# Kernel tuning notes

Measured on AMD Instinct MI355X. Metric: run time of the kernel, lower is better.

## Reference

```python
import jax, jax.numpy as jnp
import numpy as np


def setup_inputs() -> dict:
    key = jax.random.key(0)
    k1, k2, k3 = jax.random.split(key, 3)
    b, n, d, f = 16, 2048, 256, 256
    features = jax.random.normal(k1, (b, n, d), dtype=jnp.float32)
    # dense adjacency; row-normalize like MeanAggregator's normalized A
    A = jax.random.uniform(k2, (b, n, n), dtype=jnp.float32)
    A = A / jnp.sum(A, axis=-1, keepdims=True)
    weight = jax.random.normal(k3, (2 * d, f), dtype=jnp.float32) * (1.0 / np.sqrt(2 * d))
    bias = jnp.zeros((f,), dtype=jnp.float32)
    return {"features": features, "A": A, "weight": weight, "bias": bias}


def reference(features, A, weight, bias):
    # agg = A @ features  (MeanAggregator: row-normalized adjacency)
    agg = jnp.einsum('bnm,bmd->bnd', A, features)  # [b,n,d]
    d = features.shape[-1]
    # split-weight GEMM instead of materializing concat:
    # [feat, agg] @ W == feat @ W[:d] + agg @ W[d:]
    out = (jnp.einsum('bnd,df->bnf', features, weight[:d])
           + jnp.einsum('bnd,df->bnf', agg, weight[d:])
           + bias)
    return jax.nn.relu(out)
```

## Files before the change

kernel.cpp:

```cpp
#include <hip/hip_runtime.h>

typedef __attribute__((ext_vector_type(8))) short bf16x8;
typedef __attribute__((ext_vector_type(4))) float f32x4;

__device__ __forceinline__ unsigned short f2bf(float f) {
    unsigned int u = __builtin_bit_cast(unsigned int, f);
    unsigned int r = (u + 0x7FFFu + ((u >> 16) & 1u)) >> 16;
    return (unsigned short)r;
}
__device__ __forceinline__ unsigned int pkbf(float lo, float hi) {
    unsigned int ul = __builtin_bit_cast(unsigned int, lo) + 0x8000u;
    unsigned int uh = __builtin_bit_cast(unsigned int, hi) + 0x8000u;
    return (uh & 0xFFFF0000u) | (ul >> 16);
}
__device__ __forceinline__ float bf2f(unsigned short u) {
    unsigned int x = ((unsigned int)u) << 16;
    return __builtin_bit_cast(float, x);
}

__device__ __forceinline__ void gll16(const void* g, void* l) {
    __builtin_amdgcn_global_load_lds(
        (const __attribute__((address_space(1))) void*)g,
        (__attribute__((address_space(3))) void*)l, 16, 0, 0);
}

__global__ __launch_bounds__(256) void transpose_cvt_kernel(
    const float* __restrict__ src, unsigned short* __restrict__ dstT,
    unsigned short* __restrict__ dstS, int R, int C)
{
    __shared__ float tile[64][65];
    const int b = blockIdx.z;
    const float* s = src + (size_t)b * R * C;
    const int r0 = blockIdx.x * 64, c0 = blockIdx.y * 64;
    const int t = threadIdx.x;
    const int r = t >> 2, cg = (t & 3) * 16;

    float v[16];
    const float4* p = reinterpret_cast<const float4*>(s + (size_t)(r0 + r) * C + c0 + cg);
#pragma unroll
    for (int i = 0; i < 4; ++i) {
        float4 q = p[i];
        v[4 * i + 0] = q.x; v[4 * i + 1] = q.y; v[4 * i + 2] = q.z; v[4 * i + 3] = q.w;
    }
#pragma unroll
    for (int i = 0; i < 16; ++i) tile[r][cg + i] = v[i];

    if (dstS) {
        unsigned int w[8];
#pragma unroll
        for (int i = 0; i < 8; ++i)
            w[i] = (unsigned)f2bf(v[2 * i]) | ((unsigned)f2bf(v[2 * i + 1]) << 16);
        unsigned int* d = reinterpret_cast<unsigned int*>(
            dstS + (size_t)b * R * C + (size_t)(r0 + r) * C + c0 + cg);
        *reinterpret_cast<uint4*>(d)     = make_uint4(w[0], w[1], w[2], w[3]);
        *reinterpret_cast<uint4*>(d + 4) = make_uint4(w[4], w[5], w[6], w[7]);
    }

    __syncthreads();

    const int cl = t >> 2, rg = (t & 3) * 16;
    unsigned int w[8];
#pragma unroll
    for (int i = 0; i < 8; ++i) {
        unsigned short lo = f2bf(tile[rg + 2 * i][cl]);
        unsigned short hi = f2bf(tile[rg + 2 * i + 1][cl]);
        w[i] = (unsigned)lo | ((unsigned)hi << 16);
    }
    unsigned int* d = reinterpret_cast<unsigned int*>(
        dstT + (size_t)b * R * C + (size_t)(c0 + cl) * R + r0 + rg);
    *reinterpret_cast<uint4*>(d)     = make_uint4(w[0], w[1], w[2], w[3]);
    *reinterpret_cast<uint4*>(d + 4) = make_uint4(w[4], w[5], w[6], w[7]);
}

__global__ __launch_bounds__(256, 2) void kpre_gemm(
    const float* __restrict__ F, const unsigned short* __restrict__ Wt,
    const float* __restrict__ bias, unsigned short* __restrict__ H,
    unsigned short* __restrict__ Gt)
{
    __shared__ __align__(16) short Fb[64 * 256];
    __shared__ __align__(16) short Wb[256 * 64];

    const int tid = threadIdx.x;
    const int lane = tid & 63, wid = tid >> 6;
    const int lo = lane & 15, hi = lane >> 4;
    const int rb = blockIdx.x;
    const int batch = rb >> 5;
    const int mb = (rb & 31) * 64;
    const size_t m0g = (size_t)rb * 64;

    {
        const int frow = tid >> 2, fq = tid & 3;
        const float* fp = F + (m0g + frow) * 256 + fq * 64;
#pragma unroll
        for (int g = 0; g < 2; ++g) {
            float4 q[8];
#pragma unroll
            for (int i = 0; i < 8; ++i)
                q[i] = reinterpret_cast<const float4*>(fp)[g * 8 + i];
#pragma unroll
            for (int j = 0; j < 4; ++j) {
                unsigned int w0 = pkbf(q[2*j].x,   q[2*j].y);
                unsigned int w1 = pkbf(q[2*j].z,   q[2*j].w);
                unsigned int w2 = pkbf(q[2*j+1].x, q[2*j+1].y);
                unsigned int w3 = pkbf(q[2*j+1].z, q[2*j+1].w);
                int slot = fq * 8 + g * 4 + j;
                int off = frow * 256 + ((slot ^ (frow & 7)) << 3);
                *reinterpret_cast<uint4*>(&Fb[off]) = make_uint4(w0, w1, w2, w3);
            }
        }
    }

    f32x4 acc[4][4];

#pragma unroll
    for (int pass = 0; pass < 2; ++pass) {
#pragma unroll
        for (int m = 0; m < 4; ++m)
#pragma unroll
            for (int n = 0; n < 4; ++n) acc[m][n] = (f32x4){0.f, 0.f, 0.f, 0.f};

        for (int kt = 0; kt < 4; ++kt) {
            const int kbase = pass * 256 + kt * 64;
#pragma unroll
            for (int it = 0; it < 8; ++it) {
                int si = it * 256 + tid;
                int row = si >> 3, slot = si & 7;
                const unsigned short* g = Wt + (size_t)row * 512 + kbase + ((slot ^ (row & 7)) << 3);
                gll16(g, Wb + (size_t)si * 8);
            }
            __syncthreads();

#pragma unroll
            for (int kk = 0; kk < 2; ++kk) {
                bf16x8 af[4], bw[4];
#pragma unroll
                for (int m = 0; m < 4; ++m) {
                    int row = m * 16 + lo;
                    int slot = kt * 8 + kk * 4 + hi;
                    af[m] = *reinterpret_cast<const bf16x8*>(&Fb[row * 256 + ((slot ^ (row & 7)) << 3)]);
                }
#pragma unroll
                for (int n = 0; n < 4; ++n) {
                    int row = wid * 64 + n * 16 + lo;
                    bw[n] = *reinterpret_cast<const bf16x8*>(&Wb[row * 64 + (((kk * 4 + hi) ^ (row & 7)) << 3)]);
                }
#pragma unroll
                for (int m = 0; m < 4; ++m)
#pragma unroll
                    for (int n = 0; n < 4; ++n)
                        acc[m][n] = __builtin_amdgcn_mfma_f32_16x16x32_bf16(af[m], bw[n], acc[m][n], 0, 0, 0);
            }
            __syncthreads();
        }

        if (pass == 0) {
            float bv[4];
#pragma unroll
            for (int n = 0; n < 4; ++n) bv[n] = bias[wid * 64 + n * 16 + lo];
            unsigned short* Hb = H + m0g * 256;
#pragma unroll
            for (int m = 0; m < 4; ++m)
#pragma unroll
                for (int n = 0; n < 4; ++n)
#pragma unroll
                    for (int j = 0; j < 4; ++j) {
                        int row = m * 16 + hi * 4 + j;
                        int col = wid * 64 + n * 16 + lo;
                        Hb[(size_t)row * 256 + col] = f2bf(acc[m][n][j] + bv[n]);
                    }
        } else {
            short* T = Wb + wid * 4096;
#pragma unroll
            for (int m = 0; m < 4; ++m)
#pragma unroll
                for (int n = 0; n < 4; ++n)
#pragma unroll
                    for (int j = 0; j < 4; ++j) {
                        int gr = m * 16 + hi * 4 + j;
                        int gc = n * 16 + lo;
                        int slot = gr >> 3, e = gr & 7;
                        T[gc * 64 + ((slot ^ (gc & 7)) << 3) + e] = f2bf(acc[m][n][j]);
                    }
            unsigned short* Gb = Gt + ((size_t)batch * 256 + wid * 64) * 2048 + mb;
#pragma unroll
            for (int i = 0; i < 8; ++i) {
                int f = i * 8 + (lane >> 3);
                int s = lane & 7;
                bf16x8 v = *reinterpret_cast<const bf16x8*>(&T[f * 64 + ((s ^ (f & 7)) << 3)]);
                *reinterpret_cast<bf16x8*>(Gb + (size_t)f * 2048 + s * 8) = v;
            }
        }
    }
}

__global__ __launch_bounds__(512) void kmain_gemm(
    const float* __restrict__ A, const unsigned short* __restrict__ Gt,
    unsigned short* __restrict__ P)
{
    __shared__ __align__(16) short Ab[2][256 * 64];
    __shared__ __align__(16) short Bb[2][256 * 64];

    const int tid = threadIdx.x;
    const int lane = tid & 63, wid = tid >> 6;
    const int wr = wid >> 2, wc = wid & 3;
    const int lo = lane & 15, hi = lane >> 4;

    const int bid = blockIdx.x;
    const int wg = ((bid & 7) << 5) | (bid >> 3);
    const int batch = wg >> 4;
    const int ks    = (wg >> 3) & 1;
    const int mt    = wg & 7;

    const float* Abase = A + ((size_t)batch * 2048 + (size_t)mt * 256) * 2048 + (size_t)ks * 1024;
    const unsigned short* Gbase = Gt + (size_t)batch * 256 * 2048 + (size_t)ks * 1024;

    const int arow = tid >> 1;
    const int ac0  = (tid & 1) * 32;

    f32x4 acc[8][4];
#pragma unroll
    for (int m = 0; m < 8; ++m)
#pragma unroll
        for (int n = 0; n < 4; ++n) acc[m][n] = (f32x4){0.f, 0.f, 0.f, 0.f};

    float4 qa[8];
    auto loadA = [&](int k0) {
        const float4* p = reinterpret_cast<const float4*>(
            Abase + (size_t)arow * 2048 + k0 + ac0);
#pragma unroll
        for (int i = 0; i < 8; ++i) qa[i] = p[i];
    };
    auto writeA = [&](int buf) {
#pragma unroll
        for (int j = 0; j < 4; ++j) {
            uint4 w;
            w.x = pkbf(qa[2*j].x,   qa[2*j].y);
            w.y = pkbf(qa[2*j].z,   qa[2*j].w);
            w.z = pkbf(qa[2*j+1].x, qa[2*j+1].y);
            w.w = pkbf(qa[2*j+1].z, qa[2*j+1].w);
            int slot = (tid & 1) * 4 + j;
            int off = arow * 64 + ((slot ^ (arow & 7)) << 3);
            *reinterpret_cast<uint4*>(&Ab[buf][off]) = w;
        }
    };
    auto stageB = [&](int buf, int k0) {
#pragma unroll
        for (int it = 0; it < 4; ++it) {
            int si = it * 512 + tid;
            int row = si >> 3, slot = si & 7;
            const unsigned short* g = Gbase + (size_t)row * 2048 + k0 + ((slot ^ (row & 7)) << 3);
            gll16(g, &Bb[buf][(size_t)si * 8]);
        }
    };
    auto compute = [&](int buf) {
#pragma unroll
        for (int kk = 0; kk < 2; ++kk) {
            bf16x8 bfv[4];
#pragma unroll
            for (int n = 0; n < 4; ++n) {
                int row = wc * 64 + n * 16 + lo;
                bfv[n] = *reinterpret_cast<const bf16x8*>(
                    &Bb[buf][row * 64 + (((kk * 4 + hi) ^ (row & 7)) << 3)]);
            }
#pragma unroll
            for (int mh = 0; mh < 2; ++mh) {
                bf16x8 af[4];
#pragma unroll
                for (int m = 0; m < 4; ++m) {
                    int row = wr * 128 + (mh * 4 + m) * 16 + lo;
                    af[m] = *reinterpret_cast<const bf16x8*>(
                        &Ab[buf][row * 64 + (((kk * 4 + hi) ^ (row & 7)) << 3)]);
                }
                __builtin_amdgcn_s_setprio(1);
#pragma unroll
                for (int m = 0; m < 4; ++m)
#pragma unroll
                    for (int n = 0; n < 4; ++n)
                        acc[mh * 4 + m][n] = __builtin_amdgcn_mfma_f32_16x16x32_bf16(
                            af[m], bfv[n], acc[mh * 4 + m][n], 0, 0, 0);
                __builtin_amdgcn_s_setprio(0);
            }
        }
    };

    loadA(0);
    stageB(0, 0);
    writeA(0);
    __syncthreads();
    loadA(64);
    stageB(1, 64);

    for (int t = 0; t < 16; ++t) {
        const int cur = t & 1;
        compute(cur);
        if (t + 1 < 16) writeA(cur ^ 1);
        __syncthreads();
        if (t + 2 < 16) {
            loadA((t + 2) * 64);
            stageB(cur, (t + 2) * 64);
        }
    }

    unsigned short* Pb = P + ((size_t)ks * 32768 + (size_t)batch * 2048 + (size_t)mt * 256) * 256;
#pragma unroll
    for (int m = 0; m < 8; ++m) {
#pragma unroll
        for (int n = 0; n < 4; ++n) {
            int col = wc * 64 + n * 16 + lo;
#pragma unroll
            for (int j = 0; j < 4; ++j) {
                int row = wr * 128 + m * 16 + hi * 4 + j;
                Pb[(size_t)row * 256 + col] = f2bf(acc[m][n][j]);
            }
        }
    }
}

__global__ __launch_bounds__(256) void kred_kernel(
    const unsigned short* __restrict__ P, const unsigned short* __restrict__ H,
    float* __restrict__ out)
{
    const long long n8 = (long long)32768 * 256 / 8;
    const long long p1 = (long long)32768 * 256;
    long long i = (long long)blockIdx.x * 256 + threadIdx.x;
    const long long stride = (long long)gridDim.x * 256;
    for (; i < n8; i += stride) {
        bf16x8 a = *reinterpret_cast<const bf16x8*>(&P[i * 8]);
        bf16x8 b = *reinterpret_cast<const bf16x8*>(&P[p1 + i * 8]);
        bf16x8 h = *reinterpret_cast<const bf16x8*>(&H[i * 8]);
        float4 o0, o1;
        float v;
        v = bf2f((unsigned short)a[0]) + bf2f((unsigned short)b[0]) + bf2f((unsigned short)h[0]); o0.x = fmaxf(v, 0.f);
        v = bf2f((unsigned short)a[1]) + bf2f((unsigned short)b[1]) + bf2f((unsigned short)h[1]); o0.y = fmaxf(v, 0.f);
        v = bf2f((unsigned short)a[2]) + bf2f((unsigned short)b[2]) + bf2f((unsigned short)h[2]); o0.z = fmaxf(v, 0.f);
        v = bf2f((unsigned short)a[3]) + bf2f((unsigned short)b[3]) + bf2f((unsigned short)h[3]); o0.w = fmaxf(v, 0.f);
        v = bf2f((unsigned short)a[4]) + bf2f((unsigned short)b[4]) + bf2f((unsigned short)h[4]); o1.x = fmaxf(v, 0.f);
        v = bf2f((unsigned short)a[5]) + bf2f((unsigned short)b[5]) + bf2f((unsigned short)h[5]); o1.y = fmaxf(v, 0.f);
        v = bf2f((unsigned short)a[6]) + bf2f((unsigned short)b[6]) + bf2f((unsigned short)h[6]); o1.z = fmaxf(v, 0.f);
        v = bf2f((unsigned short)a[7]) + bf2f((unsigned short)b[7]) + bf2f((unsigned short)h[7]); o1.w = fmaxf(v, 0.f);
        reinterpret_cast<float4*>(out + i * 8)[0] = o0;
        reinterpret_cast<float4*>(out + i * 8)[1] = o1;
    }
}

extern "C" void kernel_launch(void* const* d_in, const int* in_sizes, int n_in,
                              void* d_out, int out_size, void* d_ws, size_t ws_size,
                              hipStream_t stream) {
    const float* features = (const float*)d_in[0];
    const float* A        = (const float*)d_in[1];
    const float* weight   = (const float*)d_in[2];
    const float* bias     = (const float*)d_in[3];
    float* out = (float*)d_out;

    const size_t WT_B = (size_t)256 * 512 * 2;
    const size_t H_B  = (size_t)32768 * 256 * 2;
    const size_t GT_B = (size_t)16 * 256 * 2048 * 2;
    const size_t P_B  = (size_t)2 * 32768 * 256 * 2;
    if (ws_size < WT_B + H_B + GT_B + P_B) return;

    char* ws = (char*)d_ws;
    unsigned short* Wt = (unsigned short*)ws;
    unsigned short* H  = (unsigned short*)(ws + WT_B);
    unsigned short* Gt = (unsigned short*)(ws + WT_B + H_B);
    unsigned short* P  = (unsigned short*)(ws + WT_B + H_B + GT_B);

    dim3 gW(512 / 64, 256 / 64, 1);
    transpose_cvt_kernel<<<gW, 256, 0, stream>>>(weight, Wt, nullptr, 512, 256);

    kpre_gemm<<<512, 256, 0, stream>>>(features, Wt, bias, H, Gt);

    kmain_gemm<<<256, 512, 0, stream>>>(A, Gt, P);

    kred_kernel<<<2048, 256, 0, stream>>>(P, H, out);
}
```

Before: 138.2 us.

## Restructure A-tile pipeline with double register buffers and manual waitcnt barriers

Changes the A-tile global load pattern so each thread reads one float4 per row across 8 rows, which gives lanes coalesced row-contiguous accesses. Register staging is double-buffered (qa0/qa1) so the next A tile is in flight while the current one computes. __syncthreads is replaced by explicit s_waitcnt vmcnt(8) plus s_barrier, letting outstanding loads overlap the barrier, and launch_bounds(512,2) is added to target two blocks per CU. Two register buffers raise register pressure, and the occupancy hint may cause spills.

```diff
diff --git a/kernel.cpp b/kernel.cpp
--- a/kernel.cpp
+++ b/kernel.cpp
@@ -193,7 +193,7 @@
     }
 }
 
-__global__ __launch_bounds__(512) void kmain_gemm(
+__global__ __launch_bounds__(512, 2) void kmain_gemm(
     const float* __restrict__ A, const unsigned short* __restrict__ Gt,
     unsigned short* __restrict__ P)
 {
@@ -214,8 +214,8 @@
     const float* Abase = A + ((size_t)batch * 2048 + (size_t)mt * 256) * 2048 + (size_t)ks * 1024;
     const unsigned short* Gbase = Gt + (size_t)batch * 256 * 2048 + (size_t)ks * 1024;
 
-    const int arow = tid >> 1;
-    const int ac0  = (tid & 1) * 32;
+    const int ar0 = tid >> 4;
+    const int as  = tid & 15;
 
     f32x4 acc[8][4];
 #pragma unroll
@@ -223,24 +223,24 @@
 #pragma unroll
         for (int n = 0; n < 4; ++n) acc[m][n] = (f32x4){0.f, 0.f, 0.f, 0.f};
 
-    float4 qa[8];
-    auto loadA = [&](int k0) {
-        const float4* p = reinterpret_cast<const float4*>(
-            Abase + (size_t)arow * 2048 + k0 + ac0);
-#pragma unroll
-        for (int i = 0; i < 8; ++i) qa[i] = p[i];
+    f32x4 qa0[8], qa1[8];
+
+    auto loadA = [&](f32x4* q, int k0) {
+        const f32x4* p4 = reinterpret_cast<const f32x4*>(Abase + k0);
+#pragma unroll
+        for (int i = 0; i < 8; ++i)
+            q[i] = p4[(size_t)(ar0 + 32 * i) * 512 + as];
     };
-    auto writeA = [&](int buf) {
-#pragma unroll
-        for (int j = 0; j < 4; ++j) {
-            uint4 w;
-            w.x = pkbf(qa[2*j].x,   qa[2*j].y);
-            w.y = pkbf(qa[2*j].z,   qa[2*j].w);
-            w.z = pkbf(qa[2*j+1].x, qa[2*j+1].y);
-            w.w = pkbf(qa[2*j+1].z, qa[2*j+1].w);
-            int slot = (tid & 1) * 4 + j;
-            int off = arow * 64 + ((slot ^ (arow & 7)) << 3);
-            *reinterpret_cast<uint4*>(&Ab[buf][off]) = w;
+    auto writeA = [&](int buf, const f32x4* q) {
+#pragma unroll
+        for (int i = 0; i < 8; ++i) {
+            int r = ar0 + 32 * i;
+            uint2 w;
+            w.x = pkbf(q[i][0], q[i][1]);
+            w.y = pkbf(q[i][2], q[i][3]);
+            int s = as >> 1;
+            int off = r * 64 + ((s ^ (r & 7)) << 3) + (as & 1) * 4;
+            *reinterpret_cast<uint2*>(&Ab[buf][off]) = w;
         }
     };
     auto stageB = [&](int buf, int k0) {
@@ -283,23 +283,38 @@
         }
     };
 
-    loadA(0);
+    loadA(qa0, 0);
     stageB(0, 0);
-    writeA(0);
-    __syncthreads();
-    loadA(64);
+    writeA(0, qa0);
+    loadA(qa1, 64);
+    asm volatile("s_waitcnt vmcnt(8) lgkmcnt(0)" ::: "memory");
+    __builtin_amdgcn_s_barrier();
+    asm volatile("" ::: "memory");
     stageB(1, 64);
 
-    for (int t = 0; t < 16; ++t) {
-        const int cur = t & 1;
-        compute(cur);
-        if (t + 1 < 16) writeA(cur ^ 1);
-        __syncthreads();
-        if (t + 2 < 16) {
-            loadA((t + 2) * 64);
-            stageB(cur, (t + 2) * 64);
-        }
-    }
+    for (int tt = 0; tt < 7; ++tt) {
+        const int t0 = tt * 2;
+        writeA(1, qa1);
+        loadA(qa0, (t0 + 2) * 64);
+        compute(0);
+        asm volatile("s_waitcnt vmcnt(8) lgkmcnt(0)" ::: "memory");
+        __builtin_amdgcn_s_barrier();
+        asm volatile("" ::: "memory");
+        stageB(0, (t0 + 2) * 64);
+        writeA(0, qa0);
+        loadA(qa1, (t0 + 3) * 64);
+        compute(1);
+        asm volatile("s_waitcnt vmcnt(8) lgkmcnt(0)" ::: "memory");
+        __builtin_amdgcn_s_barrier();
+        asm volatile("" ::: "memory");
+        stageB(1, (t0 + 3) * 64);
+    }
+    writeA(1, qa1);
+    compute(0);
+    asm volatile("s_waitcnt vmcnt(0) lgkmcnt(0)" ::: "memory");
+    __builtin_amdgcn_s_barrier();
+    asm volatile("" ::: "memory");
+    compute(1);
 
     unsigned short* Pb = P + ((size_t)ks * 32768 + (size_t)batch * 2048 + (size_t)mt * 256) * 256;
 #pragma unroll
```

Measured after the change: 125.7 us. -9.0%, faster.
